# Optimization experiments

Hardware: AMD Instinct MI355X
Metric: run time of the kernel (lower is better)

The kernel has to match this reference:

```python
import jax, jax.numpy as jnp
import numpy as np

N_VOXELS = 2_000_000
NUM_CLUSTERS = 20_000


def setup_inputs() -> dict:
    key = jax.random.key(0)
    k1, k2 = jax.random.split(key)
    data = jax.random.normal(k1, (N_VOXELS, 6), dtype=jnp.float32)
    clusts = jax.random.randint(k2, (N_VOXELS,), 0, NUM_CLUSTERS, dtype=jnp.int32)
    return {"data": data, "clusts": clusts}


def reference(data, clusts):
    # data: [N, 6]; clusts: [N] segment ids in [0, NUM_CLUSTERS)
    C = NUM_CLUSTERS
    voxels = data[:, :3]  # [N, 3]
    seg = clusts

    counts = jax.ops.segment_sum(jnp.ones((voxels.shape[0],), voxels.dtype), seg, num_segments=C)  # [C]
    center = jax.ops.segment_sum(voxels, seg, num_segments=C) / counts[:, None]  # [C, 3]

    xc = voxels - center[seg]  # centered coords, [N, 3]
    # per-cluster scatter matrix A = x^T x, [C, 3, 3]
    A = jax.ops.segment_sum(xc[:, :, None] * xc[:, None, :], seg, num_segments=C)

    # eigh returns ascending eigenvalues, same convention as torch.symeig
    w, v = jnp.linalg.eigh(A)  # w: [C, 3], v: [C, 3, 3]
    w2 = w[:, 2]
    dirwt = 1.0 - w[:, 1] / w2  # [C]
    B = A / w2[:, None, None]  # normalized scatter matrix, [C, 3, 3]
    v0 = v[:, :, 2]  # principal axis, [C, 3]

    # direction disambiguation: sc = dot(x0, ||x - x0 v0||)
    v0n = v0[seg]  # [N, 3]
    x0 = jnp.einsum('nd,nd->n', xc, v0n)  # projection onto principal axis
    xp0 = xc - x0[:, None] * v0n  # residual off-axis component
    np0 = jnp.linalg.norm(xp0, axis=1)
    sc = jax.ops.segment_sum(x0 * np0, seg, num_segments=C)  # [C]

    v0 = jnp.where(sc[:, None] < 0, -v0, v0) * dirwt[:, None]

    # features: center(3) | B flat(9) | v0(3) | size(1) -> [C, 16]
    return jnp.concatenate([center, B.reshape(C, 9), v0, counts[:, None]], axis=1)
```

## Files before the change

kernel.cpp:

```cpp
#include <hip/hip_runtime.h>
#include <hip/hip_bf16.h>
#include <math.h>

#define NVOX    2000000
#define NCLUST  20000
#define NREG    1250
#define HREG    (NREG/2)
#define CLR     16
#define CAPR    2048
#define VPB     4096
#define FS_TB   1024
#define P2TB    512
#define CAP_CL  192

struct ClustOut {
    float cx, cy, cz;
    float B[9];
    float vx, vy, vz;
    float dirwt;
    float n;
};

__device__ inline ClustOut eig_from_moments(float a0, float a1, float a2, float a3,
                                            float a4, float a5, float a6, float a7,
                                            float a8, float a9) {
    ClustOut o;
    float n  = a0;
    float inv = (n > 0.0f) ? (1.0f / n) : 0.0f;
    float cx = a1 * inv, cy = a2 * inv, cz = a3 * inv;
    float A00 = a4 - a1 * cx;
    float A01 = a5 - a1 * cy;
    float A02 = a6 - a1 * cz;
    float A11 = a7 - a2 * cy;
    float A12 = a8 - a2 * cz;
    float A22 = a9 - a3 * cz;

    float q = (A00 + A11 + A22) * (1.0f / 3.0f);
    float b00 = A00 - q, b11 = A11 - q, b22 = A22 - q;
    float p2 = b00 * b00 + b11 * b11 + b22 * b22
             + 2.0f * (A01 * A01 + A02 * A02 + A12 * A12);
    float p = sqrtf(p2 * (1.0f / 6.0f));
    float w0, w1, w2;
    if (p > 1e-30f) {
        float invp = 1.0f / p;
        float c00 = b00 * invp, c11 = b11 * invp, c22 = b22 * invp;
        float c01 = A01 * invp, c02 = A02 * invp, c12 = A12 * invp;
        float det = c00 * (c11 * c22 - c12 * c12)
                  - c01 * (c01 * c22 - c12 * c02)
                  + c02 * (c01 * c12 - c11 * c02);
        float r = 0.5f * det;
        r = fminf(1.0f, fmaxf(-1.0f, r));
        float phi = acosf(r) * (1.0f / 3.0f);
        w2 = q + 2.0f * p * cosf(phi);
        w0 = q + 2.0f * p * cosf(phi + 2.0943951023931953f);
        w1 = 3.0f * q - w2 - w0;
    } else {
        w0 = w1 = w2 = q;
    }

    float invw2 = (w2 != 0.0f) ? (1.0f / w2) : 0.0f;
    o.dirwt = 1.0f - w1 * invw2;

    float M0[9] = { A00 - w0, A01, A02,
                    A01, A11 - w0, A12,
                    A02, A12, A22 - w0 };
    float M1[9] = { A00 - w1, A01, A02,
                    A01, A11 - w1, A12,
                    A02, A12, A22 - w1 };
    float P[9];
#pragma unroll
    for (int i = 0; i < 3; ++i)
#pragma unroll
        for (int j = 0; j < 3; ++j)
            P[i * 3 + j] = M0[i * 3 + 0] * M1[0 * 3 + j]
                         + M0[i * 3 + 1] * M1[1 * 3 + j]
                         + M0[i * 3 + 2] * M1[2 * 3 + j];
    float n0 = P[0] * P[0] + P[3] * P[3] + P[6] * P[6];
    float n1 = P[1] * P[1] + P[4] * P[4] + P[7] * P[7];
    float n2 = P[2] * P[2] + P[5] * P[5] + P[8] * P[8];
    float vx, vy, vz, nn;
    if (n0 >= n1 && n0 >= n2)      { vx = P[0]; vy = P[3]; vz = P[6]; nn = n0; }
    else if (n1 >= n2)             { vx = P[1]; vy = P[4]; vz = P[7]; nn = n1; }
    else                           { vx = P[2]; vy = P[5]; vz = P[8]; nn = n2; }
    if (nn > 1e-30f) {
        float s = 1.0f / sqrtf(nn);
        vx *= s; vy *= s; vz *= s;
    } else {
        vx = vy = vz = 0.0f;
    }
    o.cx = cx; o.cy = cy; o.cz = cz;
    o.vx = vx; o.vy = vy; o.vz = vz;
    o.n = n;
    o.B[0] = A00 * invw2; o.B[1] = A01 * invw2; o.B[2] = A02 * invw2;
    o.B[3] = A01 * invw2; o.B[4] = A11 * invw2; o.B[5] = A12 * invw2;
    o.B[6] = A02 * invw2; o.B[7] = A12 * invw2; o.B[8] = A22 * invw2;
    return o;
}

__device__ inline void write_row(float* out, int c, const ClustOut& o, float score) {
    float f = (score < 0.0f) ? -o.dirwt : o.dirwt;
    float4* o4 = reinterpret_cast<float4*>(out + (size_t)c * 16);
    o4[0] = make_float4(o.cx, o.cy, o.cz, o.B[0]);
    o4[1] = make_float4(o.B[1], o.B[2], o.B[3], o.B[4]);
    o4[2] = make_float4(o.B[5], o.B[6], o.B[7], o.B[8]);
    o4[3] = make_float4(o.vx * f, o.vy * f, o.vz * f, o.n);
}


__global__ __launch_bounds__(FS_TB) void k_fscatter(const float* __restrict__ data,
                                                    const int* __restrict__ clusts,
                                                    unsigned int* __restrict__ gcnt,
                                                    float4* __restrict__ sv4, int n) {
    __shared__ unsigned int h[HREG];
    __shared__ unsigned int scn[HREG];
    __shared__ unsigned int live[NREG];
    __shared__ unsigned int dsto[NREG];
    __shared__ float4 vox[VPB];

    int t = threadIdx.x;
    int b = blockIdx.x;
    int s = b * VPB;
    int btotal = min(n - s, VPB);

    for (int w = t; w < HREG; w += FS_TB) h[w] = 0;
    __syncthreads();

    float4 r0, r1, r2, r3;
    int g0 = -1, g1 = -1, g2 = -1, g3 = -1;
    int i0 = t, i1 = i0 + FS_TB, i2 = i1 + FS_TB, i3 = i2 + FS_TB;
    if (i0 < btotal) {
        const float* d = data + (size_t)(s + i0) * 6;
        float2 xy = *reinterpret_cast<const float2*>(d);
        int c = clusts[s + i0];
        r0 = make_float4(xy.x, xy.y, d[2], __int_as_float(c));
        g0 = c >> 4;
        atomicAdd(&h[g0 >> 1], 1u << ((g0 & 1) * 16));
    }
    if (i1 < btotal) {
        const float* d = data + (size_t)(s + i1) * 6;
        float2 xy = *reinterpret_cast<const float2*>(d);
        int c = clusts[s + i1];
        r1 = make_float4(xy.x, xy.y, d[2], __int_as_float(c));
        g1 = c >> 4;
        atomicAdd(&h[g1 >> 1], 1u << ((g1 & 1) * 16));
    }
    if (i2 < btotal) {
        const float* d = data + (size_t)(s + i2) * 6;
        float2 xy = *reinterpret_cast<const float2*>(d);
        int c = clusts[s + i2];
        r2 = make_float4(xy.x, xy.y, d[2], __int_as_float(c));
        g2 = c >> 4;
        atomicAdd(&h[g2 >> 1], 1u << ((g2 & 1) * 16));
    }
    if (i3 < btotal) {
        const float* d = data + (size_t)(s + i3) * 6;
        float2 xy = *reinterpret_cast<const float2*>(d);
        int c = clusts[s + i3];
        r3 = make_float4(xy.x, xy.y, d[2], __int_as_float(c));
        g3 = c >> 4;
        atomicAdd(&h[g3 >> 1], 1u << ((g3 & 1) * 16));
    }
    __syncthreads();

    if (t < HREG) {
        unsigned int v = h[t];
        scn[t] = (v & 0xFFFFu) + (v >> 16);
    }
    __syncthreads();
    for (int off = 1; off < HREG; off <<= 1) {
        unsigned int v = (t >= off && t < HREG) ? scn[t - off] : 0u;
        __syncthreads();
        if (t < HREG) scn[t] += v;
        __syncthreads();
    }

    for (int w = t; w < NREG; w += FS_TB) {
        int wd = w >> 1;
        unsigned int packed = h[wd];
        unsigned int lo = packed & 0xFFFFu;
        unsigned int exclw = (wd == 0) ? 0u : scn[wd - 1];
        unsigned int base = exclw + ((w & 1) ? lo : 0u);
        unsigned int cntw = (w & 1) ? (packed >> 16) : lo;
        unsigned int gbase = cntw ? atomicAdd(&gcnt[w], cntw) : 0u;
        live[w] = base;
        dsto[w] = (unsigned int)w * CAPR + gbase - base;
    }
    __syncthreads();

    if (g0 >= 0) vox[atomicAdd(&live[g0], 1u)] = r0;
    if (g1 >= 0) vox[atomicAdd(&live[g1], 1u)] = r1;
    if (g2 >= 0) vox[atomicAdd(&live[g2], 1u)] = r2;
    if (g3 >= 0) vox[atomicAdd(&live[g3], 1u)] = r3;
    __syncthreads();

#pragma unroll
    for (int k = 0; k < VPB / FS_TB; ++k) {
        int i = t + k * FS_TB;
        if (i < btotal) {
            float4 v = vox[i];
            int w = __float_as_int(v.w) >> 4;
            unsigned int j = dsto[w] + (unsigned int)i;
            if (j < (unsigned int)(w + 1) * CAPR) sv4[j] = v;
        }
    }
}

__global__ __launch_bounds__(P2TB) void k_bpass2(const float4* __restrict__ sv4,
                                                 const unsigned int* __restrict__ gcnt,
                                                 float* __restrict__ out) {
    __shared__ float4 vox[CLR][CAP_CL];
    __shared__ unsigned int hc[CLR];
    int rid = blockIdx.x;
    unsigned int seg0 = (unsigned int)rid * CAPR;
    unsigned int cnt = min(gcnt[rid], (unsigned int)CAPR);
    int t = threadIdx.x, wv = t >> 6, lane = t & 63;

    if (t < CLR) hc[t] = 0;
    __syncthreads();

    for (unsigned int i = t; i < cnt; i += P2TB) {
        float4 v = sv4[seg0 + i];
        int lc = __float_as_int(v.w) & 15;
        unsigned int r = atomicAdd(&hc[lc], 1u);
        if (r < CAP_CL) vox[lc][r] = v;
    }
    __syncthreads();

#pragma unroll
    for (int k = 0; k < 2; ++k) {
        int lc = wv * 2 + k;
        unsigned int e = min(hc[lc], (unsigned int)CAP_CL);
        float a0 = 0, a1 = 0, a2 = 0, a3 = 0, a4 = 0,
              a5 = 0, a6 = 0, a7 = 0, a8 = 0, a9 = 0;
        for (unsigned int j = lane; j < e; j += 64) {
            float4 v = vox[lc][j];
            float x = v.x, y = v.y, z = v.z;
            a0 += 1.0f;
            a1 += x; a2 += y; a3 += z;
            a4 += x * x; a5 += x * y; a6 += x * z;
            a7 += y * y; a8 += y * z; a9 += z * z;
        }
#pragma unroll
        for (int m = 32; m; m >>= 1) {
            a0 += __shfl_xor(a0, m); a1 += __shfl_xor(a1, m);
            a2 += __shfl_xor(a2, m); a3 += __shfl_xor(a3, m);
            a4 += __shfl_xor(a4, m); a5 += __shfl_xor(a5, m);
            a6 += __shfl_xor(a6, m); a7 += __shfl_xor(a7, m);
            a8 += __shfl_xor(a8, m); a9 += __shfl_xor(a9, m);
        }
        ClustOut o = eig_from_moments(a0, a1, a2, a3, a4, a5, a6, a7, a8, a9);
        float sum = 0.0f;
        for (unsigned int j = lane; j < e; j += 64) {
            float4 v = vox[lc][j];
            float xcx = v.x - o.cx, xcy = v.y - o.cy, xcz = v.z - o.cz;
            float x0 = xcx * o.vx + xcy * o.vy + xcz * o.vz;
            float px = xcx - x0 * o.vx;
            float py = xcy - x0 * o.vy;
            float pz = xcz - x0 * o.vz;
            sum += x0 * sqrtf(px * px + py * py + pz * pz);
        }
#pragma unroll
        for (int m = 32; m; m >>= 1) sum += __shfl_xor(sum, m);
        if (lane == 0) write_row(out, rid * CLR + lc, o, sum);
    }
}

__global__ __launch_bounds__(256) void k_accum(const float* __restrict__ data,
                                               const int* __restrict__ clusts,
                                               float* __restrict__ mom, int n) {
    int i = blockIdx.x * blockDim.x + threadIdx.x;
    if (i >= n) return;
    const float* d = data + (size_t)i * 6;
    float2 xy = *reinterpret_cast<const float2*>(d);
    float x = xy.x, y = xy.y, z = d[2];
    int c = clusts[i];
    float* m = mom + (size_t)c * 10;
    atomicAdd(m + 0, 1.0f);
    atomicAdd(m + 1, x);
    atomicAdd(m + 2, y);
    atomicAdd(m + 3, z);
    atomicAdd(m + 4, x * x);
    atomicAdd(m + 5, x * y);
    atomicAdd(m + 6, x * z);
    atomicAdd(m + 7, y * y);
    atomicAdd(m + 8, y * z);
    atomicAdd(m + 9, z * z);
}

__global__ __launch_bounds__(256) void k_eigen(const float* __restrict__ mom,
                                               float* __restrict__ out,
                                               float* __restrict__ dirwt_ws, int C) {
    int c = blockIdx.x * blockDim.x + threadIdx.x;
    if (c >= C) return;
    const float* m = mom + (size_t)c * 10;
    ClustOut o = eig_from_moments(m[0], m[1], m[2], m[3], m[4],
                                  m[5], m[6], m[7], m[8], m[9]);
    float* p = out + (size_t)c * 16;
    p[0] = o.cx; p[1] = o.cy; p[2] = o.cz;
#pragma unroll
    for (int k = 0; k < 9; ++k) p[3 + k] = o.B[k];
    p[12] = o.vx; p[13] = o.vy; p[14] = o.vz;
    p[15] = o.n;
    dirwt_ws[c] = o.dirwt;
}

__global__ __launch_bounds__(256) void k_score(const float* __restrict__ data,
                                               const int* __restrict__ clusts,
                                               const float* __restrict__ out,
                                               float* __restrict__ sc, int n) {
    int i = blockIdx.x * blockDim.x + threadIdx.x;
    if (i >= n) return;
    const float* d = data + (size_t)i * 6;
    float2 xy = *reinterpret_cast<const float2*>(d);
    float x = xy.x, y = xy.y, z = d[2];
    int c = clusts[i];
    const float* o = out + (size_t)c * 16;
    float xcx = x - o[0], xcy = y - o[1], xcz = z - o[2];
    float vx = o[12], vy = o[13], vz = o[14];
    float x0 = xcx * vx + xcy * vy + xcz * vz;
    float px = xcx - x0 * vx;
    float py = xcy - x0 * vy;
    float pz = xcz - x0 * vz;
    atomicAdd(&sc[c], x0 * sqrtf(px * px + py * py + pz * pz));
}

__global__ __launch_bounds__(256) void k_final(const float* __restrict__ sc,
                                               const float* __restrict__ dirwt_ws,
                                               float* __restrict__ out, int C) {
    int c = blockIdx.x * blockDim.x + threadIdx.x;
    if (c >= C) return;
    float f = dirwt_ws[c];
    if (sc[c] < 0.0f) f = -f;
    float* o = out + (size_t)c * 16;
    o[12] *= f; o[13] *= f; o[14] *= f;
}

extern "C" void kernel_launch(void* const* d_in, const int* in_sizes, int n_in,
                              void* d_out, int out_size, void* d_ws, size_t ws_size,
                              hipStream_t stream) {
    const float* data  = (const float*)d_in[0];
    const int* clusts  = (const int*)d_in[1];
    float* out         = (float*)d_out;

    const int C = NCLUST;
    const int n = in_sizes[1];
    const int NB = (n + VPB - 1) / VPB;

    size_t off = 0;
    auto alloc = [&](size_t bytes) {
        size_t o = off;
        off += (bytes + 255) & ~(size_t)255;
        return o;
    };
    size_t o_gcnt = alloc((size_t)NREG * sizeof(unsigned int));
    size_t o_sv4  = alloc((size_t)NREG * CAPR * sizeof(float4));
    size_t needed = off;

    char* ws = (char*)d_ws;

    if (ws_size >= needed) {
        unsigned int* gcnt = (unsigned int*)(ws + o_gcnt);
        float4*       sv4  = (float4*)(ws + o_sv4);

        hipMemsetAsync(gcnt, 0, (size_t)NREG * sizeof(unsigned int), stream);
        k_fscatter<<<NB, FS_TB, 0, stream>>>(data, clusts, gcnt, sv4, n);
        k_bpass2<<<NREG, P2TB, 0, stream>>>(sv4, gcnt, out);
    } else {
        float* mom   = (float*)d_ws;
        float* sc    = mom + (size_t)10 * C;
        float* dirwt = sc + C;
        hipMemsetAsync(d_ws, 0, (size_t)11 * C * sizeof(float), stream);
        const int gbv = (n + 255) / 256;
        const int gbc = (C + 255) / 256;
        k_accum<<<gbv, 256, 0, stream>>>(data, clusts, mom, n);
        k_eigen<<<gbc, 256, 0, stream>>>(mom, out, dirwt, C);
        k_score<<<gbv, 256, 0, stream>>>(data, clusts, out, sc, n);
        k_final<<<gbc, 256, 0, stream>>>(sc, dirwt, out, C);
    }
}
```

Baseline: 134.3 us.

## Pack four region counters per 64-bit global atomic and reuse histogram ranks

Region counters move from one 32-bit global atomic each to four 16-bit fields packed into one 64-bit atomicAdd. The number of global atomics per block drops by four. The histogram atomics also return each voxel's rank, so the second pass of shared-memory atomics for the local scatter is gone. The cost is that 16-bit global counts can overflow if a region ever gets more than 65535 voxels (expected about 1600 here), and one barrier between the dsto writes and the vox writes is removed.

```diff
diff --git a/kernel.cpp b/kernel.cpp
--- a/kernel.cpp
+++ b/kernel.cpp
@@ -5,6 +5,8 @@
 #define NVOX    2000000
 #define NCLUST  20000
 #define NREG    1250
+#define NREGP   1252
+#define G4      (NREGP/4)
 #define HREG    (NREG/2)
 #define CLR     16
 #define CAPR    2048
@@ -109,12 +111,12 @@
 
 __global__ __launch_bounds__(FS_TB) void k_fscatter(const float* __restrict__ data,
                                                     const int* __restrict__ clusts,
-                                                    unsigned int* __restrict__ gcnt,
+                                                    unsigned long long* __restrict__ gcnt64,
                                                     float4* __restrict__ sv4, int n) {
-    __shared__ unsigned int h[HREG];
+    __shared__ unsigned int live[NREGP];
     __shared__ unsigned int scn[HREG];
-    __shared__ unsigned int live[NREG];
-    __shared__ unsigned int dsto[NREG];
+    __shared__ unsigned short base[NREGP];
+    __shared__ unsigned int dsto[NREGP];
     __shared__ float4 vox[VPB];
 
     int t = threadIdx.x;
@@ -122,11 +124,12 @@
     int s = b * VPB;
     int btotal = min(n - s, VPB);
 
-    for (int w = t; w < HREG; w += FS_TB) h[w] = 0;
+    for (int w = t; w < NREGP; w += FS_TB) live[w] = 0;
     __syncthreads();
 
     float4 r0, r1, r2, r3;
     int g0 = -1, g1 = -1, g2 = -1, g3 = -1;
+    unsigned int k0 = 0, k1 = 0, k2 = 0, k3 = 0;
     int i0 = t, i1 = i0 + FS_TB, i2 = i1 + FS_TB, i3 = i2 + FS_TB;
     if (i0 < btotal) {
         const float* d = data + (size_t)(s + i0) * 6;
@@ -134,7 +137,7 @@
         int c = clusts[s + i0];
         r0 = make_float4(xy.x, xy.y, d[2], __int_as_float(c));
         g0 = c >> 4;
-        atomicAdd(&h[g0 >> 1], 1u << ((g0 & 1) * 16));
+        k0 = atomicAdd(&live[g0], 1u);
     }
     if (i1 < btotal) {
         const float* d = data + (size_t)(s + i1) * 6;
@@ -142,7 +145,7 @@
         int c = clusts[s + i1];
         r1 = make_float4(xy.x, xy.y, d[2], __int_as_float(c));
         g1 = c >> 4;
-        atomicAdd(&h[g1 >> 1], 1u << ((g1 & 1) * 16));
+        k1 = atomicAdd(&live[g1], 1u);
     }
     if (i2 < btotal) {
         const float* d = data + (size_t)(s + i2) * 6;
@@ -150,7 +153,7 @@
         int c = clusts[s + i2];
         r2 = make_float4(xy.x, xy.y, d[2], __int_as_float(c));
         g2 = c >> 4;
-        atomicAdd(&h[g2 >> 1], 1u << ((g2 & 1) * 16));
+        k2 = atomicAdd(&live[g2], 1u);
     }
     if (i3 < btotal) {
         const float* d = data + (size_t)(s + i3) * 6;
@@ -158,39 +161,43 @@
         int c = clusts[s + i3];
         r3 = make_float4(xy.x, xy.y, d[2], __int_as_float(c));
         g3 = c >> 4;
-        atomicAdd(&h[g3 >> 1], 1u << ((g3 & 1) * 16));
-    }
-    __syncthreads();
-
-    if (t < HREG) {
-        unsigned int v = h[t];
-        scn[t] = (v & 0xFFFFu) + (v >> 16);
-    }
+        k3 = atomicAdd(&live[g3], 1u);
+    }
+    __syncthreads();
+
+    if (t < HREG) scn[t] = live[2 * t] + live[2 * t + 1];
     __syncthreads();
     for (int off = 1; off < HREG; off <<= 1) {
-        unsigned int v = (t >= off && t < HREG) ? scn[t - off] : 0u;
+        unsigned int v = (t < HREG && t >= off) ? scn[t - off] : 0u;
         __syncthreads();
         if (t < HREG) scn[t] += v;
         __syncthreads();
     }
-
-    for (int w = t; w < NREG; w += FS_TB) {
-        int wd = w >> 1;
-        unsigned int packed = h[wd];
-        unsigned int lo = packed & 0xFFFFu;
-        unsigned int exclw = (wd == 0) ? 0u : scn[wd - 1];
-        unsigned int base = exclw + ((w & 1) ? lo : 0u);
-        unsigned int cntw = (w & 1) ? (packed >> 16) : lo;
-        unsigned int gbase = cntw ? atomicAdd(&gcnt[w], cntw) : 0u;
-        live[w] = base;
-        dsto[w] = (unsigned int)w * CAPR + gbase - base;
-    }
-    __syncthreads();
-
-    if (g0 >= 0) vox[atomicAdd(&live[g0], 1u)] = r0;
-    if (g1 >= 0) vox[atomicAdd(&live[g1], 1u)] = r1;
-    if (g2 >= 0) vox[atomicAdd(&live[g2], 1u)] = r2;
-    if (g3 >= 0) vox[atomicAdd(&live[g3], 1u)] = r3;
+    for (int w = t; w < NREGP; w += FS_TB) {
+        int pr = w >> 1;
+        unsigned int excl = (pr == 0) ? 0u : scn[pr - 1];
+        if (pr >= HREG) excl = scn[HREG - 1];
+        base[w] = (unsigned short)(excl + ((w & 1) ? live[w - 1] : 0u));
+    }
+    __syncthreads();
+
+    for (int g = t; g < G4; g += FS_TB) {
+        int w = g * 4;
+        unsigned long long c0 = live[w], c1 = live[w + 1],
+                           c2 = live[w + 2], c3 = live[w + 3];
+        unsigned long long add = c0 | (c1 << 16) | (c2 << 32) | (c3 << 48);
+        unsigned long long old = add ? atomicAdd(&gcnt64[g], add) : 0ull;
+#pragma unroll
+        for (int j = 0; j < 4; ++j) {
+            unsigned int gb = (unsigned int)((old >> (16 * j)) & 0xFFFFull);
+            dsto[w + j] = (unsigned int)(w + j) * CAPR + gb - (unsigned int)base[w + j];
+        }
+    }
+
+    if (g0 >= 0) vox[base[g0] + k0] = r0;
+    if (g1 >= 0) vox[base[g1] + k1] = r1;
+    if (g2 >= 0) vox[base[g2] + k2] = r2;
+    if (g3 >= 0) vox[base[g3] + k3] = r3;
     __syncthreads();
 
 #pragma unroll
@@ -206,13 +213,13 @@
 }
 
 __global__ __launch_bounds__(P2TB) void k_bpass2(const float4* __restrict__ sv4,
-                                                 const unsigned int* __restrict__ gcnt,
+                                                 const unsigned short* __restrict__ gcnt16,
                                                  float* __restrict__ out) {
     __shared__ float4 vox[CLR][CAP_CL];
     __shared__ unsigned int hc[CLR];
     int rid = blockIdx.x;
     unsigned int seg0 = (unsigned int)rid * CAPR;
-    unsigned int cnt = min(gcnt[rid], (unsigned int)CAPR);
+    unsigned int cnt = min((unsigned int)gcnt16[rid], (unsigned int)CAPR);
     int t = threadIdx.x, wv = t >> 6, lane = t & 63;
 
     if (t < CLR) hc[t] = 0;
@@ -352,19 +359,19 @@
         off += (bytes + 255) & ~(size_t)255;
         return o;
     };
-    size_t o_gcnt = alloc((size_t)NREG * sizeof(unsigned int));
+    size_t o_gcnt = alloc((size_t)G4 * sizeof(unsigned long long));
     size_t o_sv4  = alloc((size_t)NREG * CAPR * sizeof(float4));
     size_t needed = off;
 
     char* ws = (char*)d_ws;
 
     if (ws_size >= needed) {
-        unsigned int* gcnt = (unsigned int*)(ws + o_gcnt);
-        float4*       sv4  = (float4*)(ws + o_sv4);
-
-        hipMemsetAsync(gcnt, 0, (size_t)NREG * sizeof(unsigned int), stream);
-        k_fscatter<<<NB, FS_TB, 0, stream>>>(data, clusts, gcnt, sv4, n);
-        k_bpass2<<<NREG, P2TB, 0, stream>>>(sv4, gcnt, out);
+        unsigned long long* gcnt64 = (unsigned long long*)(ws + o_gcnt);
+        float4*             sv4    = (float4*)(ws + o_sv4);
+
+        hipMemsetAsync(gcnt64, 0, (size_t)G4 * sizeof(unsigned long long), stream);
+        k_fscatter<<<NB, FS_TB, 0, stream>>>(data, clusts, gcnt64, sv4, n);
+        k_bpass2<<<NREG, P2TB, 0, stream>>>(sv4, (const unsigned short*)gcnt64, out);
     } else {
         float* mom   = (float*)d_ws;
         float* sc    = mom + (size_t)10 * C;
```

Measured after the change: 132.3 us. No clear change (-1.5%).
